# Optimization experiments

Measured on AMD Instinct MI355X. Metric: run time of the kernel, lower is better.

Reference implementation:

```python
import jax, jax.numpy as jnp
import numpy as np

KERNEL = 7
PAD = 3


def setup_inputs() -> dict:
    key = jax.random.key(0)
    k1, k2 = jax.random.split(key)
    x = jax.random.normal(k1, (32, 256, 112, 112), dtype=jnp.float32)
    # Conv2d(2, 1, 7, bias=False) weight, OIHW
    W = jax.random.normal(k2, (1, 2, KERNEL, KERNEL), dtype=jnp.float32) * 0.1
    return {"x": x, "W": W}


def reference(x, W):
    # channel-wise mean and max -> [B, 2, H, W]
    avg_out = jnp.mean(x, axis=1, keepdims=True)
    max_out = jnp.max(x, axis=1, keepdims=True)
    pooled = jnp.concatenate([avg_out, max_out], axis=1)
    # 2->1 conv, padding 3 (SAME for k=7)
    y = jax.lax.conv_general_dilated(
        pooled, W,
        window_strides=(1, 1),
        padding=[(PAD, PAD), (PAD, PAD)],
        dimension_numbers=("NCHW", "OIHW", "NCHW"),
    )
    return jax.nn.sigmoid(y)
```

## Files before the change

### kernel.cpp

```cpp
#include <hip/hip_runtime.h>
#include <math.h>

#define BATCH 32
#define CH    256
#define HH    112
#define WW    112
#define HW    (HH * WW)
#define HW4   (HW / 4)

#define CHUNK 448

__global__ __launch_bounds__(448) void sa_pool_kernel(
    const float4* __restrict__ x4,
    float4* __restrict__ avg4,
    float4* __restrict__ max4)
{
    int tid = threadIdx.x;
    int b   = blockIdx.y;
    int q   = blockIdx.x * CHUNK + tid;

    const float4* p = x4 + (size_t)b * (CH * HW4) + q;

    float4 s = make_float4(0.f, 0.f, 0.f, 0.f);
    float4 m = make_float4(-INFINITY, -INFINITY, -INFINITY, -INFINITY);

    #pragma unroll 8
    for (int c = 0; c < CH; ++c) {
        float4 v = p[(size_t)c * HW4];
        s.x += v.x; s.y += v.y; s.z += v.z; s.w += v.w;
        m.x = fmaxf(m.x, v.x);
        m.y = fmaxf(m.y, v.y);
        m.z = fmaxf(m.z, v.z);
        m.w = fmaxf(m.w, v.w);
    }

    const float inv = 1.0f / (float)CH;
    float4 a = make_float4(s.x * inv, s.y * inv, s.z * inv, s.w * inv);

    int g = b * HW4 + q;
    avg4[g] = a;
    max4[g] = m;
}

#define TILE 16
#define TW   (TILE + 6)

__global__ __launch_bounds__(256) void sa_conv_kernel(
    const float* __restrict__ avgp,
    const float* __restrict__ maxp,
    const float* __restrict__ wt,
    float* __restrict__ out)
{
    __shared__ float t0[TW][TW];
    __shared__ float t1[TW][TW];
    __shared__ float w[2][49];

    int tid = threadIdx.x;
    int b   = blockIdx.z;
    int ty0 = blockIdx.y * TILE;
    int tx0 = blockIdx.x * TILE;

    if (tid < 98) w[tid / 49][tid % 49] = wt[tid];

    const float* ap = avgp + b * HW;
    const float* mp = maxp + b * HW;

    for (int idx = tid; idx < TW * TW; idx += 256) {
        int iy = idx / TW;
        int ix = idx - iy * TW;
        int gy = ty0 + iy - 3;
        int gx = tx0 + ix - 3;
        bool ok = (gy >= 0) && (gy < HH) && (gx >= 0) && (gx < WW);
        int gofs = gy * WW + gx;
        t0[iy][ix] = ok ? ap[gofs] : 0.0f;
        t1[iy][ix] = ok ? mp[gofs] : 0.0f;
    }
    __syncthreads();

    int oy = tid >> 4;
    int ox = tid & 15;

    float acc = 0.0f;
    #pragma unroll
    for (int i = 0; i < 7; ++i) {
        #pragma unroll
        for (int j = 0; j < 7; ++j) {
            acc += w[0][i * 7 + j] * t0[oy + i][ox + j];
            acc += w[1][i * 7 + j] * t1[oy + i][ox + j];
        }
    }

    float y = 1.0f / (1.0f + expf(-acc));
    out[b * HW + (ty0 + oy) * WW + (tx0 + ox)] = y;
}

extern "C" void kernel_launch(void* const* d_in, const int* in_sizes, int n_in,
                              void* d_out, int out_size, void* d_ws, size_t ws_size,
                              hipStream_t stream)
{
    const float* x  = (const float*)d_in[0];
    const float* wt = (const float*)d_in[1];
    float* out = (float*)d_out;

    float* avgp = (float*)d_ws;
    float* maxp = avgp + (size_t)BATCH * HW;

    dim3 grid1(HW4 / CHUNK, BATCH);
    sa_pool_kernel<<<grid1, CHUNK, 0, stream>>>(
        (const float4*)x, (float4*)avgp, (float4*)maxp);

    dim3 grid2(WW / TILE, HH / TILE, BATCH);
    sa_conv_kernel<<<grid2, 256, 0, stream>>>(avgp, maxp, wt, out);
}
```

Before: 83.76 us.

## Split channel reduction into groups with partial sums combined in conv kernel

The pooling stage is reorganised so that each block reduces one group of 32 channels for a whole image. Each thread keeps seven float4 accumulators, which gives it more independent loads in flight. The per-group partial sums and maxima are written to the workspace, and the conv kernel combines them while it builds its shared-memory tile. This trades more workspace traffic and a heavier tile load for more parallelism in the bandwidth-bound reduction. The original two-kernel path stays as a fallback when the workspace is too small.

```diff
diff --git a/kernel.cpp b/kernel.cpp
--- a/kernel.cpp
+++ b/kernel.cpp
@@ -8,9 +8,114 @@
 #define HW    (HH * WW)
 #define HW4   (HW / 4)
 
+#define NG    8
+#define CPG   (CH / NG)
+#define PT    448
+#define KK    (HW4 / PT)
+
+__global__ __launch_bounds__(PT) void sa_pool_part_kernel(
+    const float4* __restrict__ x4,
+    float4* __restrict__ sum_part,
+    float4* __restrict__ max_part)
+{
+    int tid = threadIdx.x;
+    int b   = blockIdx.x;
+    int g   = blockIdx.y;
+
+    const float4* p = x4 + ((size_t)b * CH + (size_t)g * CPG) * HW4;
+
+    float4 s[KK], m[KK];
+    #pragma unroll
+    for (int k = 0; k < KK; ++k) {
+        s[k] = make_float4(0.f, 0.f, 0.f, 0.f);
+        m[k] = make_float4(-INFINITY, -INFINITY, -INFINITY, -INFINITY);
+    }
+
+    #pragma unroll 2
+    for (int c = 0; c < CPG; ++c) {
+        const float4* pc = p + (size_t)c * HW4 + tid;
+        #pragma unroll
+        for (int k = 0; k < KK; ++k) {
+            float4 v = pc[k * PT];
+            s[k].x += v.x; s[k].y += v.y; s[k].z += v.z; s[k].w += v.w;
+            m[k].x = fmaxf(m[k].x, v.x);
+            m[k].y = fmaxf(m[k].y, v.y);
+            m[k].z = fmaxf(m[k].z, v.z);
+            m[k].w = fmaxf(m[k].w, v.w);
+        }
+    }
+
+    float4* so = sum_part + ((size_t)g * BATCH + b) * HW4 + tid;
+    float4* mo = max_part + ((size_t)g * BATCH + b) * HW4 + tid;
+    #pragma unroll
+    for (int k = 0; k < KK; ++k) {
+        so[k * PT] = s[k];
+        mo[k * PT] = m[k];
+    }
+}
+
+#define TILE 16
+#define TW   (TILE + 6)
+
+__global__ __launch_bounds__(256) void sa_conv_comb_kernel(
+    const float* __restrict__ sum_part,
+    const float* __restrict__ max_part,
+    const float* __restrict__ wt,
+    float* __restrict__ out)
+{
+    __shared__ float t0[TW][TW];
+    __shared__ float t1[TW][TW];
+    __shared__ float w[2][49];
+
+    int tid = threadIdx.x;
+    int b   = blockIdx.z;
+    int ty0 = blockIdx.y * TILE;
+    int tx0 = blockIdx.x * TILE;
+
+    if (tid < 98) w[tid / 49][tid % 49] = wt[tid];
+
+    const float inv = 1.0f / (float)CH;
+
+    for (int idx = tid; idx < TW * TW; idx += 256) {
+        int iy = idx / TW;
+        int ix = idx - iy * TW;
+        int gy = ty0 + iy - 3;
+        int gx = tx0 + ix - 3;
+        bool ok = (gy >= 0) && (gy < HH) && (gx >= 0) && (gx < WW);
+        float ssum = 0.f, mmax = -INFINITY;
+        if (ok) {
+            size_t gofs = (size_t)b * HW + gy * WW + gx;
+            #pragma unroll
+            for (int g = 0; g < NG; ++g) {
+                ssum += sum_part[(size_t)g * (BATCH * HW) + gofs];
+                mmax = fmaxf(mmax, max_part[(size_t)g * (BATCH * HW) + gofs]);
+            }
+        }
+        t0[iy][ix] = ok ? ssum * inv : 0.f;
+        t1[iy][ix] = ok ? mmax : 0.f;
+    }
+    __syncthreads();
+
+    int oy = tid >> 4;
+    int ox = tid & 15;
+
+    float acc = 0.0f;
+    #pragma unroll
+    for (int i = 0; i < 7; ++i) {
+        #pragma unroll
+        for (int j = 0; j < 7; ++j) {
+            acc += w[0][i * 7 + j] * t0[oy + i][ox + j];
+            acc += w[1][i * 7 + j] * t1[oy + i][ox + j];
+        }
+    }
+
+    float y = 1.0f / (1.0f + expf(-acc));
+    out[b * HW + (ty0 + oy) * WW + (tx0 + ox)] = y;
+}
+
 #define CHUNK 448
 
-__global__ __launch_bounds__(448) void sa_pool_kernel(
+__global__ __launch_bounds__(448) void sa_pool_kernel_fb(
     const float4* __restrict__ x4,
     float4* __restrict__ avg4,
     float4* __restrict__ max4)
@@ -42,10 +147,7 @@
     max4[g] = m;
 }
 
-#define TILE 16
-#define TW   (TILE + 6)
-
-__global__ __launch_bounds__(256) void sa_conv_kernel(
+__global__ __launch_bounds__(256) void sa_conv_kernel_fb(
     const float* __restrict__ avgp,
     const float* __restrict__ maxp,
     const float* __restrict__ wt,
@@ -102,13 +204,28 @@
     const float* wt = (const float*)d_in[1];
     float* out = (float*)d_out;
 
-    float* avgp = (float*)d_ws;
-    float* maxp = avgp + (size_t)BATCH * HW;
-
-    dim3 grid1(HW4 / CHUNK, BATCH);
-    sa_pool_kernel<<<grid1, CHUNK, 0, stream>>>(
-        (const float4*)x, (float4*)avgp, (float4*)maxp);
-
-    dim3 grid2(WW / TILE, HH / TILE, BATCH);
-    sa_conv_kernel<<<grid2, 256, 0, stream>>>(avgp, maxp, wt, out);
-}
+    const size_t plane_elems = (size_t)BATCH * HW;
+    const size_t need = (size_t)NG * plane_elems * sizeof(float) * 2;
+
+    if (ws_size >= need) {
+        float* sum_part = (float*)d_ws;
+        float* max_part = sum_part + (size_t)NG * plane_elems;
+
+        dim3 grid1(BATCH, NG);
+        sa_pool_part_kernel<<<grid1, PT, 0, stream>>>(
+            (const float4*)x, (float4*)sum_part, (float4*)max_part);
+
+        dim3 grid2(WW / TILE, HH / TILE, BATCH);
+        sa_conv_comb_kernel<<<grid2, 256, 0, stream>>>(sum_part, max_part, wt, out);
+    } else {
+        float* avgp = (float*)d_ws;
+        float* maxp = avgp + plane_elems;
+
+        dim3 grid1(HW4 / CHUNK, BATCH);
+        sa_pool_kernel_fb<<<grid1, CHUNK, 0, stream>>>(
+            (const float4*)x, (float4*)avgp, (float4*)maxp);
+
+        dim3 grid2(WW / TILE, HH / TILE, BATCH);
+        sa_conv_kernel_fb<<<grid2, 256, 0, stream>>>(avgp, maxp, wt, out);
+    }
+}
```

Result: slower. 113.2 us (+35.2%).
